# Performance work log

Measured on AMD Instinct MI355X. Metric: run time of the kernel, lower is better.

## Reference

```python
import jax, jax.numpy as jnp
import numpy as np

B, S, D, H = 2, 4096, 512, 8
DK = D // H
LN_EPS = 1e-5


def setup_inputs() -> dict:
    key = jax.random.key(0)
    ks = jax.random.split(key, 12)
    lim = 1.0 / np.sqrt(D)
    inp = {
        "query": jax.random.normal(ks[0], (B, S, D), jnp.float32),
        "key_in": jax.random.normal(ks[1], (B, S, D), jnp.float32),
        "value": jax.random.normal(ks[2], (B, S, D), jnp.float32),
        # causal mask: positions with 0 are masked out (masked_fill(mask == 0, -1e9))
        "mask": jnp.broadcast_to(jnp.tril(jnp.ones((S, S), jnp.int32)), (B, S, S)),
        "Wq": jax.random.uniform(ks[3], (D, D), jnp.float32, -lim, lim),
        "bq": jnp.zeros((D,), jnp.float32),
        "Wk": jax.random.uniform(ks[4], (D, D), jnp.float32, -lim, lim),
        "bk": jnp.zeros((D,), jnp.float32),
        "Wv": jax.random.uniform(ks[5], (D, D), jnp.float32, -lim, lim),
        "bv": jnp.zeros((D,), jnp.float32),
        "Wo": jax.random.uniform(ks[6], (D, D), jnp.float32, -lim, lim),
        "bo": jnp.zeros((D,), jnp.float32),
        "ln_gamma": jnp.ones((D,), jnp.float32),
        "ln_beta": jnp.zeros((D,), jnp.float32),
    }
    return inp


def _split_heads(x):
    # [B, S, D] -> [B, H, S, DK]
    return x.reshape(B, S, H, DK).transpose(0, 2, 1, 3)


def reference(query, key_in, value, mask, Wq, bq, Wk, bk, Wv, bv, Wo, bo, ln_gamma, ln_beta):
    residual = query
    q = _split_heads(query @ Wq.T + bq)
    k = _split_heads(key_in @ Wk.T + bk)
    v = _split_heads(value @ Wv.T + bv)

    scores = jnp.einsum("bhqd,bhkd->bhqk", q, k) / jnp.sqrt(jnp.float32(DK))
    scores = jnp.where(mask[:, None, :, :] == 0, jnp.float32(-1e9), scores)
    attn = jax.nn.softmax(scores, axis=-1)  # dropout is identity in eval mode
    out = jnp.einsum("bhqk,bhkd->bhqd", attn, v)

    out = out.transpose(0, 2, 1, 3).reshape(B, S, D)
    out = out @ Wo.T + bo

    x = out + residual
    mu = jnp.mean(x, axis=-1, keepdims=True)
    var = jnp.mean(jnp.square(x - mu), axis=-1, keepdims=True)
    return (x - mu) * jax.lax.rsqrt(var + LN_EPS) * ln_gamma + ln_beta
```

## Files before the change

### kernel.cpp

```cpp
#include <hip/hip_runtime.h>
#include <hip/hip_bf16.h>

#define B_ 2
#define S_ 4096
#define D_ 512
#define H_ 8
#define DK_ 64

typedef short short8_t __attribute__((ext_vector_type(8)));
typedef short short4_t __attribute__((ext_vector_type(4)));
typedef float float4_t __attribute__((ext_vector_type(4)));

__device__ __forceinline__ short f2bf(float f) {
    union { float f; unsigned u; } c; c.f = f;
    unsigned r = c.u + 0x7FFFu + ((c.u >> 16) & 1u);
    return (short)(r >> 16);
}

#define MFMA32(a, b, c) __builtin_amdgcn_mfma_f32_16x16x32_bf16((a), (b), (c), 0, 0, 0)

#if __has_builtin(__builtin_amdgcn_mfma_f32_16x16x16bf16_1k)
__device__ __forceinline__ float4_t MFMA16(short4_t a, short4_t b, float4_t c) {
    return __builtin_amdgcn_mfma_f32_16x16x16bf16_1k(a, b, c, 0, 0, 0);
}
#else
__device__ __forceinline__ float4_t MFMA16(short4_t a, short4_t b, float4_t c) {
    asm volatile("v_mfma_f32_16x16x16_bf16 %0, %1, %2, %0" : "+v"(c) : "v"(a), "v"(b));
    return c;
}
#endif

__device__ __forceinline__ void gll16(const void* g, const void* l) {
    __builtin_amdgcn_global_load_lds(
        (__attribute__((address_space(1))) void*)(g),
        (__attribute__((address_space(3))) void*)(l), 16, 0, 0);
}

__global__ __launch_bounds__(256) void convert_all(
    const float* __restrict__ q, const float* __restrict__ k, const float* __restrict__ v,
    const float* __restrict__ Wq, const float* __restrict__ Wk,
    const float* __restrict__ Wv, const float* __restrict__ Wo,
    short* __restrict__ Xq, short* __restrict__ Xk, short* __restrict__ Xv,
    short* __restrict__ Wbf)
{
    const int XN = (B_ * S_ * D_) / 8;
    int gid = blockIdx.x * 256 + threadIdx.x;
    const float* src;
    short8_t* dst;
    int off;
    if (gid < 3 * XN) {
        int z = gid >> 19;
        off = gid & (XN - 1);
        src = (z == 0) ? q : (z == 1) ? k : v;
        dst = (short8_t*)((z == 0) ? Xq : (z == 1) ? Xk : Xv);
    } else {
        int g2 = gid - 3 * XN;
        int z = g2 >> 15;
        off = g2 & 32767;
        src = (z == 0) ? Wq : (z == 1) ? Wk : (z == 2) ? Wv : Wo;
        dst = (short8_t*)(Wbf + z * (D_ * D_));
    }
    float4_t f0 = ((const float4_t*)src)[off * 2];
    float4_t f1 = ((const float4_t*)src)[off * 2 + 1];
    short8_t o = { f2bf(f0[0]), f2bf(f0[1]), f2bf(f0[2]), f2bf(f0[3]),
                   f2bf(f1[0]), f2bf(f1[1]), f2bf(f1[2]), f2bf(f1[3]) };
    dst[off] = o;
}

__global__ __launch_bounds__(256) void gemm_qkv(
    const short* __restrict__ Xq, const short* __restrict__ Xk, const short* __restrict__ Xv,
    const short* __restrict__ Wbf,
    const float* __restrict__ bq, const float* __restrict__ bk, const float* __restrict__ bv,
    short* __restrict__ Qs, short* __restrict__ Ks, short* __restrict__ Vt)
{
    __shared__ short sA[128 * 64];
    __shared__ short sB[128 * 64];

    const int z = blockIdx.z;
    const short* X    = (z == 0) ? Xq : (z == 1) ? Xk : Xv;
    const short* W    = Wbf + z * (D_ * D_);
    const float* bias = (z == 0) ? bq : (z == 1) ? bk : bv;

    const int col0 = blockIdx.x * 128, row0 = blockIdx.y * 128;
    const int tid = threadIdx.x, w = tid >> 6, l = tid & 63;
    const int lr = l & 15, lg = l >> 4;
    const int wm = w >> 1, wn = w & 1;
    const int srow = l >> 3, sch = l & 7;

    float4_t acc[4][4];
    #pragma unroll
    for (int i = 0; i < 4; i++)
        #pragma unroll
        for (int j = 0; j < 4; j++)
            acc[i][j] = (float4_t){0.f, 0.f, 0.f, 0.f};

    for (int k0 = 0; k0 < D_; k0 += 64) {
        #pragma unroll
        for (int rnd = 0; rnd < 4; rnd++) {
            int r = rnd * 32 + w * 8 + srow;
            gll16(X + (row0 + r) * D_ + k0 + (sch ^ (r & 7)) * 8, &sA[(rnd * 32 + w * 8) * 64]);
            gll16(W + (col0 + r) * D_ + k0 + (sch ^ (r & 7)) * 8, &sB[(rnd * 32 + w * 8) * 64]);
        }
        __syncthreads();
        short8_t a[4], bb[4];
        #pragma unroll
        for (int kk = 0; kk < 2; kk++) {
            #pragma unroll
            for (int i = 0; i < 4; i++) {
                int rw = wm * 64 + i * 16 + lr;
                a[i] = *(const short8_t*)(&sA[rw * 64 + (((kk * 4 + lg) ^ (lr & 7)) * 8)]);
            }
            #pragma unroll
            for (int j = 0; j < 4; j++) {
                int rw = wn * 64 + j * 16 + lr;
                bb[j] = *(const short8_t*)(&sB[rw * 64 + (((kk * 4 + lg) ^ (lr & 7)) * 8)]);
            }
            if (z < 2) {
                #pragma unroll
                for (int i = 0; i < 4; i++)
                    #pragma unroll
                    for (int j = 0; j < 4; j++)
                        acc[i][j] = MFMA32(bb[j], a[i], acc[i][j]);
            } else {
                #pragma unroll
                for (int i = 0; i < 4; i++)
                    #pragma unroll
                    for (int j = 0; j < 4; j++)
                        acc[i][j] = MFMA32(a[i], bb[j], acc[i][j]);
            }
        }
        __syncthreads();
    }

    if (z < 2) {
        short* Out = (z == 0) ? Qs : Ks;
        #pragma unroll
        for (int j = 0; j < 4; j++) {
            int colb = col0 + wn * 64 + j * 16 + lg * 4;
            int h = colb >> 6, dk = colb & 63;
            float4_t b4 = *(const float4_t*)(bias + colb);
            #pragma unroll
            for (int i = 0; i < 4; i++) {
                int s = row0 + wm * 64 + i * 16 + lr;
                short4_t o4 = { f2bf(acc[i][j][0] + b4[0]), f2bf(acc[i][j][1] + b4[1]),
                                f2bf(acc[i][j][2] + b4[2]), f2bf(acc[i][j][3] + b4[3]) };
                *(short4_t*)(Out + (((s >> 12) * H_ + h) * S_ + (s & 4095)) * 64 + dk) = o4;
            }
        }
    } else {
        #pragma unroll
        for (int j = 0; j < 4; j++) {
            int dkg = col0 + wn * 64 + j * 16 + lr;
            int h = dkg >> 6, dk = dkg & 63;
            float bv_ = bias[dkg];
            #pragma unroll
            for (int i = 0; i < 4; i++) {
                int s0 = row0 + wm * 64 + i * 16 + lg * 4;
                short4_t o4 = { f2bf(acc[i][j][0] + bv_), f2bf(acc[i][j][1] + bv_),
                                f2bf(acc[i][j][2] + bv_), f2bf(acc[i][j][3] + bv_) };
                *(short4_t*)(Vt + (((s0 >> 12) * H_ + h) * 64 + dk) * S_ + (s0 & 4095)) = o4;
            }
        }
    }
}

#define SCALE_LOG2 0.1803368801111244f

__global__ __launch_bounds__(256) void attn_kernel(
    const short* __restrict__ Qs, const short* __restrict__ Ks,
    const short* __restrict__ Vt, short* __restrict__ Og)
{
    __shared__ float smem[8192];
    short* sKb = (short*)smem;
    short* sVb = (short*)smem + 8192;

    const int v = blockIdx.x;
    const int bh = (v & 7) * 2 + ((v >> 3) & 1);
    const int qt = 127 - (v >> 4);
    const int b = bh >> 3, h = bh & 7;
    const int tid = threadIdx.x, w = tid >> 6, l = tid & 63;
    const int lr = l & 15, lg = l >> 4;
    const int qbase = qt * 32;
    const int kvT = qt / 2 + 1;
    const short* Kb = Ks + bh * (S_ * 64);
    const short* Vb = Vt + bh * (64 * S_);
    const short* Qb = Qs + bh * (S_ * 64);
    const int srow = l >> 3, sch = l & 7;

    short8_t qf[2][2];
    #pragma unroll
    for (int qb = 0; qb < 2; qb++)
        #pragma unroll
        for (int kk = 0; kk < 2; kk++)
            qf[qb][kk] = *(const short8_t*)(Qb + (qbase + qb * 16 + lr) * 64 + kk * 32 + lg * 8);

    float m_run[2] = {-1e30f, -1e30f}, l_run[2] = {0.f, 0.f};
    float4_t O[2][4];
    #pragma unroll
    for (int qb = 0; qb < 2; qb++)
        #pragma unroll
        for (int nj = 0; nj < 4; nj++)
            O[qb][nj] = (float4_t){0.f, 0.f, 0.f, 0.f};

    auto STAGE = [&](int t, int bi) {
        #pragma unroll
        for (int rnd = 0; rnd < 2; rnd++) {
            int r = rnd * 32 + w * 8 + srow;
            gll16(Kb + (t * 64 + r) * 64 + (sch ^ (r & 7)) * 8, sKb + bi * 4096 + (rnd * 32 + w * 8) * 64);
            gll16(Vb + r * S_ + t * 64 + (sch ^ (r & 7)) * 8,   sVb + bi * 4096 + (rnd * 32 + w * 8) * 64);
        }
    };

    STAGE(0, 0);
    for (int t = 0; t < kvT; t++) {
        int cur = t & 1;
        if (t + 1 < kvT) {
            STAGE(t + 1, cur ^ 1);
            asm volatile("s_waitcnt vmcnt(4)" ::: "memory");
        } else {
            asm volatile("s_waitcnt vmcnt(0)" ::: "memory");
        }
        __builtin_amdgcn_s_barrier();
        __builtin_amdgcn_sched_barrier(0);

        const int kv0 = t * 64 + w * 16;
        if (kv0 <= qbase + 16) {
            const short* K_ = sKb + cur * 4096;
            const short* V_ = sVb + cur * 4096;

            short8_t kf[2];
            #pragma unroll
            for (int kk = 0; kk < 2; kk++)
                kf[kk] = *(const short8_t*)(&K_[(w * 16 + lr) * 64 + (((kk * 4 + lg) ^ (lr & 7)) * 8)]);

            __builtin_amdgcn_s_setprio(1);
            float4_t st0 = (float4_t){0.f, 0.f, 0.f, 0.f}, st1 = st0;
            st0 = MFMA32(kf[0], qf[0][0], st0);
            st1 = MFMA32(kf[0], qf[1][0], st1);
            st0 = MFMA32(kf[1], qf[0][1], st0);
            st1 = MFMA32(kf[1], qf[1][1], st1);
            __builtin_amdgcn_s_setprio(0);

            const bool act0 = (kv0 <= qbase);
            const bool diag0 = (kv0 == qbase);
            const bool diag1 = (kv0 == qbase + 16);
            short4_t pb[2];

            #pragma unroll
            for (int qb = 0; qb < 2; qb++) {
                if (qb == 0 && !act0) continue;
                float4_t sx = qb ? st1 : st0;
                bool dg = qb ? diag1 : diag0;
                float sval[4];
                #pragma unroll
                for (int r = 0; r < 4; r++) {
                    float vv = sx[r] * SCALE_LOG2;
                    if (dg && (lg * 4 + r > lr)) vv = -1e30f;
                    sval[r] = vv;
                }
                float mx = fmaxf(fmaxf(sval[0], sval[1]), fmaxf(sval[2], sval[3]));
                mx = fmaxf(mx, __shfl_xor(mx, 16));
                mx = fmaxf(mx, __shfl_xor(mx, 32));
                float mnew = fmaxf(m_run[qb], mx);
                float al = __builtin_exp2f(m_run[qb] - mnew);
                m_run[qb] = mnew;
                float rs = 0.f;
                #pragma unroll
                for (int r = 0; r < 4; r++) {
                    float e = __builtin_exp2f(sval[r] - mnew);
                    sval[r] = e;
                    rs += e;
                }
                rs += __shfl_xor(rs, 16);
                rs += __shfl_xor(rs, 32);
                l_run[qb] = l_run[qb] * al + rs;
                #pragma unroll
                for (int nj = 0; nj < 4; nj++) O[qb][nj] *= al;
                pb[qb] = (short4_t){ f2bf(sval[0]), f2bf(sval[1]), f2bf(sval[2]), f2bf(sval[3]) };
            }

            __builtin_amdgcn_s_setprio(1);
            #pragma unroll
            for (int njd = 0; njd < 4; njd++) {
                short4_t va = *(const short4_t*)(
                    &V_[(njd * 16 + lr) * 64 + (((w * 2 + (lg >> 1)) ^ (lr & 7)) * 8) + (lg & 1) * 4]);
                if (act0) O[0][njd] = MFMA16(va, pb[0], O[0][njd]);
                O[1][njd] = MFMA16(va, pb[1], O[1][njd]);
            }
            __builtin_amdgcn_s_setprio(0);
        }
        __builtin_amdgcn_s_barrier();
        __builtin_amdgcn_sched_barrier(0);
    }

    float* sml = smem;
    if (lg == 0) {
        #pragma unroll
        for (int qb = 0; qb < 2; qb++) {
            sml[((w * 2 + qb) * 16 + lr) * 2 + 0] = m_run[qb];
            sml[((w * 2 + qb) * 16 + lr) * 2 + 1] = l_run[qb];
        }
    }
    __syncthreads();
    float fac[2];
    #pragma unroll
    for (int qb = 0; qb < 2; qb++) {
        float mw[4], lw[4];
        #pragma unroll
        for (int ww = 0; ww < 4; ww++) {
            mw[ww] = sml[((ww * 2 + qb) * 16 + lr) * 2 + 0];
            lw[ww] = sml[((ww * 2 + qb) * 16 + lr) * 2 + 1];
        }
        float mmax = fmaxf(fmaxf(mw[0], mw[1]), fmaxf(mw[2], mw[3]));
        float lsum = 0.f;
        #pragma unroll
        for (int ww = 0; ww < 4; ww++) lsum += __builtin_exp2f(mw[ww] - mmax) * lw[ww];
        fac[qb] = __builtin_exp2f(m_run[qb] - mmax) / lsum;
    }
    __syncthreads();
    float* rg = smem + w * 2048;
    #pragma unroll
    for (int qb = 0; qb < 2; qb++) {
        #pragma unroll
        for (int njd = 0; njd < 4; njd++) {
            int row = qb * 16 + lr;
            int c = (njd * 4 + lg) ^ (lr & 7);
            float4_t val = O[qb][njd] * fac[qb];
            *(float4_t*)(rg + row * 64 + c * 4) = val;
        }
    }
    __syncthreads();
    {
        int qq = tid >> 3, a = tid & 7;
        int key = qq & 7;
        float4_t s0 = (float4_t){0.f, 0.f, 0.f, 0.f}, s1 = s0;
        #pragma unroll
        for (int ww = 0; ww < 4; ww++) {
            const float* r_ = smem + ww * 2048 + qq * 64;
            s0 += *(const float4_t*)(r_ + ((a * 2) ^ key) * 4);
            s1 += *(const float4_t*)(r_ + ((a * 2 + 1) ^ key) * 4);
        }
        short8_t o8 = { f2bf(s0[0]), f2bf(s0[1]), f2bf(s0[2]), f2bf(s0[3]),
                        f2bf(s1[0]), f2bf(s1[1]), f2bf(s1[2]), f2bf(s1[3]) };
        *(short8_t*)(Og + (b * S_ + qbase + qq) * D_ + h * 64 + a * 8) = o8;
    }
}

__global__ __launch_bounds__(256) void gemm_oproj(
    const short* __restrict__ Ag, const short* __restrict__ Wbf,
    const float* __restrict__ bo, float* __restrict__ Og)
{
    __shared__ short sA[128 * 64];
    __shared__ short sB[128 * 64];

    const int col0 = blockIdx.x * 128, row0 = blockIdx.y * 128;
    const int tid = threadIdx.x, w = tid >> 6, l = tid & 63;
    const int lr = l & 15, lg = l >> 4;
    const int wm = w >> 1, wn = w & 1;
    const int srow = l >> 3, sch = l & 7;

    float4_t acc[4][4];
    #pragma unroll
    for (int i = 0; i < 4; i++)
        #pragma unroll
        for (int j = 0; j < 4; j++)
            acc[i][j] = (float4_t){0.f, 0.f, 0.f, 0.f};

    for (int k0 = 0; k0 < D_; k0 += 64) {
        #pragma unroll
        for (int rnd = 0; rnd < 4; rnd++) {
            int r = rnd * 32 + w * 8 + srow;
            gll16(Ag  + (row0 + r) * D_ + k0 + (sch ^ (r & 7)) * 8, &sA[(rnd * 32 + w * 8) * 64]);
            gll16(Wbf + (col0 + r) * D_ + k0 + (sch ^ (r & 7)) * 8, &sB[(rnd * 32 + w * 8) * 64]);
        }
        __syncthreads();
        #pragma unroll
        for (int kk = 0; kk < 2; kk++) {
            short8_t a[4], bb[4];
            #pragma unroll
            for (int i = 0; i < 4; i++) {
                int rw = wm * 64 + i * 16 + lr;
                a[i] = *(const short8_t*)(&sA[rw * 64 + (((kk * 4 + lg) ^ (lr & 7)) * 8)]);
            }
            #pragma unroll
            for (int j = 0; j < 4; j++) {
                int rw = wn * 64 + j * 16 + lr;
                bb[j] = *(const short8_t*)(&sB[rw * 64 + (((kk * 4 + lg) ^ (lr & 7)) * 8)]);
            }
            #pragma unroll
            for (int i = 0; i < 4; i++)
                #pragma unroll
                for (int j = 0; j < 4; j++)
                    acc[i][j] = MFMA32(bb[j], a[i], acc[i][j]);
        }
        __syncthreads();
    }

    #pragma unroll
    for (int j = 0; j < 4; j++) {
        int colb = col0 + wn * 64 + j * 16 + lg * 4;
        float4_t b4 = *(const float4_t*)(bo + colb);
        #pragma unroll
        for (int i = 0; i < 4; i++) {
            int s = row0 + wm * 64 + i * 16 + lr;
            float4_t o4 = acc[i][j] + b4;
            *(float4_t*)(Og + s * D_ + colb) = o4;
        }
    }
}

__global__ __launch_bounds__(128) void ln_kernel(
    const float* __restrict__ Oin, const float* __restrict__ resid,
    const float* __restrict__ gamma, const float* __restrict__ beta,
    float* __restrict__ out)
{
    __shared__ float red[4];
    const int row = blockIdx.x, tid = threadIdx.x;
    float4_t o  = *(const float4_t*)(Oin   + row * 512 + tid * 4);
    float4_t rq = *(const float4_t*)(resid + row * 512 + tid * 4);
    float4_t x = o + rq;
    float s1 = x[0] + x[1] + x[2] + x[3];
    float s2 = x[0]*x[0] + x[1]*x[1] + x[2]*x[2] + x[3]*x[3];
    #pragma unroll
    for (int m = 1; m < 64; m <<= 1) {
        s1 += __shfl_xor(s1, m, 64);
        s2 += __shfl_xor(s2, m, 64);
    }
    const int wv = tid >> 6;
    if ((tid & 63) == 0) { red[wv * 2] = s1; red[wv * 2 + 1] = s2; }
    __syncthreads();
    s1 = red[0] + red[2];
    s2 = red[1] + red[3];
    float mu  = s1 * (1.f / 512.f);
    float var = s2 * (1.f / 512.f) - mu * mu;
    float rstd = rsqrtf(var + 1e-5f);
    float4_t g  = *(const float4_t*)(gamma + tid * 4);
    float4_t be = *(const float4_t*)(beta  + tid * 4);
    float4_t y;
    #pragma unroll
    for (int c = 0; c < 4; c++) y[c] = (x[c] - mu) * rstd * g[c] + be[c];
    *(float4_t*)(out + row * 512 + tid * 4) = y;
}

extern "C" void kernel_launch(void* const* d_in, const int* in_sizes, int n_in,
                              void* d_out, int out_size, void* d_ws, size_t ws_size,
                              hipStream_t stream) {
    const float* q     = (const float*)d_in[0];
    const float* kin   = (const float*)d_in[1];
    const float* vin   = (const float*)d_in[2];
    const float* Wq    = (const float*)d_in[4];
    const float* bq    = (const float*)d_in[5];
    const float* Wk    = (const float*)d_in[6];
    const float* bk    = (const float*)d_in[7];
    const float* Wv    = (const float*)d_in[8];
    const float* bv    = (const float*)d_in[9];
    const float* Wo    = (const float*)d_in[10];
    const float* bo    = (const float*)d_in[11];
    const float* gamma = (const float*)d_in[12];
    const float* beta  = (const float*)d_in[13];
    float* out = (float*)d_out;

    char* ws = (char*)d_ws;
    short* Wbf  = (short*)(ws);
    short* Xq   = (short*)(ws + 2097152);
    short* Xk   = (short*)(ws + 10485760);
    short* Xv   = (short*)(ws + 18874368);
    short* Qs   = (short*)(ws + 27262976);
    short* Ks   = (short*)(ws + 35651584);
    short* Vt   = (short*)(ws + 44040192);
    short* Attn = (short*)(ws + 18874368);
    float* Oprj = (float*)(ws + 2097152);

    convert_all<<<6656, 256, 0, stream>>>(q, kin, vin, Wq, Wk, Wv, Wo, Xq, Xk, Xv, Wbf);
    gemm_qkv<<<dim3(4, 64, 3), 256, 0, stream>>>(Xq, Xk, Xv, Wbf, bq, bk, bv, Qs, Ks, Vt);
    attn_kernel<<<2048, 256, 0, stream>>>(Qs, Ks, Vt, Attn);
    gemm_oproj<<<dim3(4, 64), 256, 0, stream>>>(Attn, Wbf + 3 * D_ * D_, bo, Oprj);
    ln_kernel<<<8192, 128, 0, stream>>>(Oprj, q, gamma, beta, out);
}
```

Measured before the change: 418.2 us.

## Double-buffer GEMMs, fold softmax scale into Wq, lazy rescale, MFMA row sums

The QKV and output-projection GEMMs get double-buffered LDS staging with explicit vmcnt waits, so global loads overlap MFMA work. The softmax scale is folded into the Wq conversion and the Q bias, which removes a per-score multiply in attention. Attention now rescales only when the running max grows by more than a threshold, moves the masking after the exponential, and computes row sums with an MFMA against a vector of ones instead of shuffles. All bf16 conversions use the packed v_cvt_pk_bf16_f32 instruction. The trade-offs are double the LDS per GEMM block, which can lower occupancy, and slightly different numerics from the lazy rescale.

Result: faster. 394.8 us (-5.6%).

```diff
diff --git a/kernel.cpp b/kernel.cpp
--- a/kernel.cpp
+++ b/kernel.cpp
@@ -7,15 +7,19 @@
 #define H_ 8
 #define DK_ 64
 
+#define SCALE_LOG2 0.1803368801111244f
+
 typedef short short8_t __attribute__((ext_vector_type(8)));
 typedef short short4_t __attribute__((ext_vector_type(4)));
 typedef float float4_t __attribute__((ext_vector_type(4)));
 
-__device__ __forceinline__ short f2bf(float f) {
-    union { float f; unsigned u; } c; c.f = f;
-    unsigned r = c.u + 0x7FFFu + ((c.u >> 16) & 1u);
-    return (short)(r >> 16);
-}
+__device__ __forceinline__ unsigned cvtpk(float a, float b) {
+    unsigned r;
+    asm("v_cvt_pk_bf16_f32 %0, %1, %2" : "=v"(r) : "v"(a), "v"(b));
+    return r;
+}
+union PU2 { unsigned u[2]; short4_t s4; };
+union PU4 { unsigned u[4]; short8_t s8; };
 
 #define MFMA32(a, b, c) __builtin_amdgcn_mfma_f32_16x16x32_bf16((a), (b), (c), 0, 0, 0)
 
@@ -48,6 +52,7 @@
     const float* src;
     short8_t* dst;
     int off;
+    float sc = 1.f;
     if (gid < 3 * XN) {
         int z = gid >> 19;
         off = gid & (XN - 1);
@@ -59,12 +64,16 @@
         off = g2 & 32767;
         src = (z == 0) ? Wq : (z == 1) ? Wk : (z == 2) ? Wv : Wo;
         dst = (short8_t*)(Wbf + z * (D_ * D_));
-    }
-    float4_t f0 = ((const float4_t*)src)[off * 2];
-    float4_t f1 = ((const float4_t*)src)[off * 2 + 1];
-    short8_t o = { f2bf(f0[0]), f2bf(f0[1]), f2bf(f0[2]), f2bf(f0[3]),
-                   f2bf(f1[0]), f2bf(f1[1]), f2bf(f1[2]), f2bf(f1[3]) };
-    dst[off] = o;
+        if (z == 0) sc = SCALE_LOG2;
+    }
+    float4_t f0 = ((const float4_t*)src)[off * 2] * sc;
+    float4_t f1 = ((const float4_t*)src)[off * 2 + 1] * sc;
+    PU4 o;
+    o.u[0] = cvtpk(f0[0], f0[1]);
+    o.u[1] = cvtpk(f0[2], f0[3]);
+    o.u[2] = cvtpk(f1[0], f1[1]);
+    o.u[3] = cvtpk(f1[2], f1[3]);
+    dst[off] = o.s8;
 }
 
 __global__ __launch_bounds__(256) void gemm_qkv(
@@ -73,8 +82,8 @@
     const float* __restrict__ bq, const float* __restrict__ bk, const float* __restrict__ bv,
     short* __restrict__ Qs, short* __restrict__ Ks, short* __restrict__ Vt)
 {
-    __shared__ short sA[128 * 64];
-    __shared__ short sB[128 * 64];
+    __shared__ short sA[2][128 * 64];
+    __shared__ short sB[2][128 * 64];
 
     const int z = blockIdx.z;
     const short* X    = (z == 0) ? Xq : (z == 1) ? Xk : Xv;
@@ -94,26 +103,41 @@
         for (int j = 0; j < 4; j++)
             acc[i][j] = (float4_t){0.f, 0.f, 0.f, 0.f};
 
-    for (int k0 = 0; k0 < D_; k0 += 64) {
+    auto STAGE = [&](int k0, int bi) {
         #pragma unroll
         for (int rnd = 0; rnd < 4; rnd++) {
             int r = rnd * 32 + w * 8 + srow;
-            gll16(X + (row0 + r) * D_ + k0 + (sch ^ (r & 7)) * 8, &sA[(rnd * 32 + w * 8) * 64]);
-            gll16(W + (col0 + r) * D_ + k0 + (sch ^ (r & 7)) * 8, &sB[(rnd * 32 + w * 8) * 64]);
-        }
-        __syncthreads();
+            gll16(X + (row0 + r) * D_ + k0 + (sch ^ (r & 7)) * 8, &sA[bi][(rnd * 32 + w * 8) * 64]);
+            gll16(W + (col0 + r) * D_ + k0 + (sch ^ (r & 7)) * 8, &sB[bi][(rnd * 32 + w * 8) * 64]);
+        }
+    };
+
+    STAGE(0, 0);
+    for (int ks = 0; ks < 8; ks++) {
+        int cur = ks & 1;
+        if (ks < 7) {
+            STAGE((ks + 1) * 64, cur ^ 1);
+            asm volatile("s_waitcnt vmcnt(8)" ::: "memory");
+        } else {
+            asm volatile("s_waitcnt vmcnt(0)" ::: "memory");
+        }
+        __builtin_amdgcn_s_barrier();
+        __builtin_amdgcn_sched_barrier(0);
+
+        const short* pA = sA[cur];
+        const short* pB = sB[cur];
         short8_t a[4], bb[4];
         #pragma unroll
         for (int kk = 0; kk < 2; kk++) {
             #pragma unroll
             for (int i = 0; i < 4; i++) {
                 int rw = wm * 64 + i * 16 + lr;
-                a[i] = *(const short8_t*)(&sA[rw * 64 + (((kk * 4 + lg) ^ (lr & 7)) * 8)]);
+                a[i] = *(const short8_t*)(&pA[rw * 64 + (((kk * 4 + lg) ^ (lr & 7)) * 8)]);
             }
             #pragma unroll
             for (int j = 0; j < 4; j++) {
                 int rw = wn * 64 + j * 16 + lr;
-                bb[j] = *(const short8_t*)(&sB[rw * 64 + (((kk * 4 + lg) ^ (lr & 7)) * 8)]);
+                bb[j] = *(const short8_t*)(&pB[rw * 64 + (((kk * 4 + lg) ^ (lr & 7)) * 8)]);
             }
             if (z < 2) {
                 #pragma unroll
@@ -129,7 +153,8 @@
                         acc[i][j] = MFMA32(a[i], bb[j], acc[i][j]);
             }
         }
-        __syncthreads();
+        __builtin_amdgcn_s_barrier();
+        __builtin_amdgcn_sched_barrier(0);
     }
 
     if (z < 2) {
@@ -139,12 +164,14 @@
             int colb = col0 + wn * 64 + j * 16 + lg * 4;
             int h = colb >> 6, dk = colb & 63;
             float4_t b4 = *(const float4_t*)(bias + colb);
+            if (z == 0) b4 *= SCALE_LOG2;
             #pragma unroll
             for (int i = 0; i < 4; i++) {
                 int s = row0 + wm * 64 + i * 16 + lr;
-                short4_t o4 = { f2bf(acc[i][j][0] + b4[0]), f2bf(acc[i][j][1] + b4[1]),
-                                f2bf(acc[i][j][2] + b4[2]), f2bf(acc[i][j][3] + b4[3]) };
-                *(short4_t*)(Out + (((s >> 12) * H_ + h) * S_ + (s & 4095)) * 64 + dk) = o4;
+                PU2 o;
+                o.u[0] = cvtpk(acc[i][j][0] + b4[0], acc[i][j][1] + b4[1]);
+                o.u[1] = cvtpk(acc[i][j][2] + b4[2], acc[i][j][3] + b4[3]);
+                *(short4_t*)(Out + (((s >> 12) * H_ + h) * S_ + (s & 4095)) * 64 + dk) = o.s4;
             }
         }
     } else {
@@ -156,15 +183,14 @@
             #pragma unroll
             for (int i = 0; i < 4; i++) {
                 int s0 = row0 + wm * 64 + i * 16 + lg * 4;
-                short4_t o4 = { f2bf(acc[i][j][0] + bv_), f2bf(acc[i][j][1] + bv_),
-                                f2bf(acc[i][j][2] + bv_), f2bf(acc[i][j][3] + bv_) };
-                *(short4_t*)(Vt + (((s0 >> 12) * H_ + h) * 64 + dk) * S_ + (s0 & 4095)) = o4;
-            }
-        }
-    }
-}
-
-#define SCALE_LOG2 0.1803368801111244f
+                PU2 o;
+                o.u[0] = cvtpk(acc[i][j][0] + bv_, acc[i][j][1] + bv_);
+                o.u[1] = cvtpk(acc[i][j][2] + bv_, acc[i][j][3] + bv_);
+                *(short4_t*)(Vt + (((s0 >> 12) * H_ + h) * 64 + dk) * S_ + (s0 & 4095)) = o.s4;
+            }
+        }
+    }
+}
 
 __global__ __launch_bounds__(256) void attn_kernel(
     const short* __restrict__ Qs, const short* __restrict__ Ks,
@@ -186,6 +212,7 @@
     const short* Vb = Vt + bh * (64 * S_);
     const short* Qb = Qs + bh * (S_ * 64);
     const int srow = l >> 3, sch = l & 7;
+    const short4_t ones = { (short)0x3F80, (short)0x3F80, (short)0x3F80, (short)0x3F80 };
 
     short8_t qf[2][2];
     #pragma unroll
@@ -194,13 +221,16 @@
         for (int kk = 0; kk < 2; kk++)
             qf[qb][kk] = *(const short8_t*)(Qb + (qbase + qb * 16 + lr) * 64 + kk * 32 + lg * 8);
 
-    float m_run[2] = {-1e30f, -1e30f}, l_run[2] = {0.f, 0.f};
+    float m_run[2] = {-1e30f, -1e30f};
+    float4_t Lacc[2];
     float4_t O[2][4];
     #pragma unroll
-    for (int qb = 0; qb < 2; qb++)
+    for (int qb = 0; qb < 2; qb++) {
+        Lacc[qb] = (float4_t){0.f, 0.f, 0.f, 0.f};
         #pragma unroll
         for (int nj = 0; nj < 4; nj++)
             O[qb][nj] = (float4_t){0.f, 0.f, 0.f, 0.f};
+    }
 
     auto STAGE = [&](int t, int bi) {
         #pragma unroll
@@ -251,35 +281,35 @@
                 if (qb == 0 && !act0) continue;
                 float4_t sx = qb ? st1 : st0;
                 bool dg = qb ? diag1 : diag0;
-                float sval[4];
-                #pragma unroll
-                for (int r = 0; r < 4; r++) {
-                    float vv = sx[r] * SCALE_LOG2;
-                    if (dg && (lg * 4 + r > lr)) vv = -1e30f;
-                    sval[r] = vv;
-                }
-                float mx = fmaxf(fmaxf(sval[0], sval[1]), fmaxf(sval[2], sval[3]));
+                float mx = fmaxf(fmaxf(sx[0], sx[1]), fmaxf(sx[2], sx[3]));
                 mx = fmaxf(mx, __shfl_xor(mx, 16));
                 mx = fmaxf(mx, __shfl_xor(mx, 32));
-                float mnew = fmaxf(m_run[qb], mx);
-                float al = __builtin_exp2f(m_run[qb] - mnew);
-                m_run[qb] = mnew;
-                float rs = 0.f;
+                if (__any(mx > m_run[qb] + 8.f)) {
+                    float mnew = fmaxf(m_run[qb], mx);
+                    float al = __builtin_exp2f(m_run[qb] - mnew);
+                    m_run[qb] = mnew;
+                    #pragma unroll
+                    for (int nj = 0; nj < 4; nj++) O[qb][nj] *= al;
+                    Lacc[qb] *= al;
+                }
+                float e[4];
                 #pragma unroll
-                for (int r = 0; r < 4; r++) {
-                    float e = __builtin_exp2f(sval[r] - mnew);
-                    sval[r] = e;
-                    rs += e;
+                for (int r = 0; r < 4; r++)
+                    e[r] = __builtin_exp2f(sx[r] - m_run[qb]);
+                if (dg) {
+                    #pragma unroll
+                    for (int r = 0; r < 4; r++)
+                        if (lg * 4 + r > lr) e[r] = 0.f;
                 }
-                rs += __shfl_xor(rs, 16);
-                rs += __shfl_xor(rs, 32);
-                l_run[qb] = l_run[qb] * al + rs;
-                #pragma unroll
-                for (int nj = 0; nj < 4; nj++) O[qb][nj] *= al;
-                pb[qb] = (short4_t){ f2bf(sval[0]), f2bf(sval[1]), f2bf(sval[2]), f2bf(sval[3]) };
+                PU2 pu;
+                pu.u[0] = cvtpk(e[0], e[1]);
+                pu.u[1] = cvtpk(e[2], e[3]);
+                pb[qb] = pu.s4;
             }
 
             __builtin_amdgcn_s_setprio(1);
+            if (act0) Lacc[0] = MFMA16(ones, pb[0], Lacc[0]);
+            Lacc[1] = MFMA16(ones, pb[1], Lacc[1]);
             #pragma unroll
             for (int njd = 0; njd < 4; njd++) {
                 short4_t va = *(const short4_t*)(
@@ -298,7 +328,7 @@
         #pragma unroll
         for (int qb = 0; qb < 2; qb++) {
             sml[((w * 2 + qb) * 16 + lr) * 2 + 0] = m_run[qb];
-            sml[((w * 2 + qb) * 16 + lr) * 2 + 1] = l_run[qb];
+            sml[((w * 2 + qb) * 16 + lr) * 2 + 1] = Lacc[qb][0];
         }
     }
     __syncthreads();
@@ -340,9 +370,12 @@
             s0 += *(const float4_t*)(r_ + ((a * 2) ^ key) * 4);
             s1 += *(const float4_t*)(r_ + ((a * 2 + 1) ^ key) * 4);
         }
-        short8_t o8 = { f2bf(s0[0]), f2bf(s0[1]), f2bf(s0[2]), f2bf(s0[3]),
-                        f2bf(s1[0]), f2bf(s1[1]), f2bf(s1[2]), f2bf(s1[3]) };
-        *(short8_t*)(Og + (b * S_ + qbase + qq) * D_ + h * 64 + a * 8) = o8;
+        PU4 o;
+        o.u[0] = cvtpk(s0[0], s0[1]);
+        o.u[1] = cvtpk(s0[2], s0[3]);
+        o.u[2] = cvtpk(s1[0], s1[1]);
+        o.u[3] = cvtpk(s1[2], s1[3]);
+        *(short8_t*)(Og + (b * S_ + qbase + qq) * D_ + h * 64 + a * 8) = o.s8;
     }
 }
 
@@ -350,8 +383,8 @@
     const short* __restrict__ Ag, const short* __restrict__ Wbf,
     const float* __restrict__ bo, float* __restrict__ Og)
 {
-    __shared__ short sA[128 * 64];
-    __shared__ short sB[128 * 64];
+    __shared__ short sA[2][128 * 64];
+    __shared__ short sB[2][128 * 64];
 
     const int col0 = blockIdx.x * 128, row0 = blockIdx.y * 128;
     const int tid = threadIdx.x, w = tid >> 6, l = tid & 63;
@@ -366,26 +399,41 @@
         for (int j = 0; j < 4; j++)
             acc[i][j] = (float4_t){0.f, 0.f, 0.f, 0.f};
 
-    for (int k0 = 0; k0 < D_; k0 += 64) {
+    auto STAGE = [&](int k0, int bi) {
         #pragma unroll
         for (int rnd = 0; rnd < 4; rnd++) {
             int r = rnd * 32 + w * 8 + srow;
-            gll16(Ag  + (row0 + r) * D_ + k0 + (sch ^ (r & 7)) * 8, &sA[(rnd * 32 + w * 8) * 64]);
-            gll16(Wbf + (col0 + r) * D_ + k0 + (sch ^ (r & 7)) * 8, &sB[(rnd * 32 + w * 8) * 64]);
-        }
-        __syncthreads();
+            gll16(Ag  + (row0 + r) * D_ + k0 + (sch ^ (r & 7)) * 8, &sA[bi][(rnd * 32 + w * 8) * 64]);
+            gll16(Wbf + (col0 + r) * D_ + k0 + (sch ^ (r & 7)) * 8, &sB[bi][(rnd * 32 + w * 8) * 64]);
+        }
+    };
+
+    STAGE(0, 0);
+    for (int ks = 0; ks < 8; ks++) {
+        int cur = ks & 1;
+        if (ks < 7) {
+            STAGE((ks + 1) * 64, cur ^ 1);
+            asm volatile("s_waitcnt vmcnt(8)" ::: "memory");
+        } else {
+            asm volatile("s_waitcnt vmcnt(0)" ::: "memory");
+        }
+        __builtin_amdgcn_s_barrier();
+        __builtin_amdgcn_sched_barrier(0);
+
+        const short* pA = sA[cur];
+        const short* pB = sB[cur];
         #pragma unroll
         for (int kk = 0; kk < 2; kk++) {
             short8_t a[4], bb[4];
             #pragma unroll
             for (int i = 0; i < 4; i++) {
                 int rw = wm * 64 + i * 16 + lr;
-                a[i] = *(const short8_t*)(&sA[rw * 64 + (((kk * 4 + lg) ^ (lr & 7)) * 8)]);
+                a[i] = *(const short8_t*)(&pA[rw * 64 + (((kk * 4 + lg) ^ (lr & 7)) * 8)]);
             }
             #pragma unroll
             for (int j = 0; j < 4; j++) {
                 int rw = wn * 64 + j * 16 + lr;
-                bb[j] = *(const short8_t*)(&sB[rw * 64 + (((kk * 4 + lg) ^ (lr & 7)) * 8)]);
+                bb[j] = *(const short8_t*)(&pB[rw * 64 + (((kk * 4 + lg) ^ (lr & 7)) * 8)]);
             }
             #pragma unroll
             for (int i = 0; i < 4; i++)
@@ -393,7 +441,8 @@
                 for (int j = 0; j < 4; j++)
                     acc[i][j] = MFMA32(bb[j], a[i], acc[i][j]);
         }
-        __syncthreads();
+        __builtin_amdgcn_s_barrier();
+        __builtin_amdgcn_sched_barrier(0);
     }
 
     #pragma unroll
```
